# Kernel optimization log

Hardware: AMD Instinct MI355X
Metric: run time of the kernel (lower is better)

## Reference

```python
import jax, jax.numpy as jnp
import numpy as np

D_MODEL = 256
MLP_DIM = 1024
EPS = 1e-5

def _layernorm(x, g, b):
    mu = jnp.mean(x, axis=-1, keepdims=True)
    var = jnp.mean(jnp.square(x - mu), axis=-1, keepdims=True)
    return (x - mu) * jax.lax.rsqrt(var + EPS) * g + b

def setup_inputs() -> dict:
    key = jax.random.key(0)
    ks = jax.random.split(key, 4)
    d, m = D_MODEL, MLP_DIM
    x = jax.random.normal(ks[0], (8, 1024, 4, d), dtype=jnp.float32)
    w_qkv = jax.random.normal(ks[1], (3 * d, d), dtype=jnp.float32) * 0.05  # torch Linear weight (out,in)
    gamma1 = jnp.ones((d,), jnp.float32)
    beta1 = jnp.zeros((d,), jnp.float32)
    gamma2 = jnp.ones((d,), jnp.float32)
    beta2 = jnp.zeros((d,), jnp.float32)
    w1 = jax.random.normal(ks[2], (m, d), dtype=jnp.float32) * 0.05
    b1 = jnp.zeros((m,), jnp.float32)
    w2 = jax.random.normal(ks[3], (d, m), dtype=jnp.float32) * 0.05
    b2 = jnp.zeros((d,), jnp.float32)
    return {"x": x, "w_qkv": w_qkv, "gamma1": gamma1, "beta1": beta1,
            "gamma2": gamma2, "beta2": beta2, "w1": w1, "b1": b1, "w2": w2, "b2": b2}

def reference(x, w_qkv, gamma1, beta1, gamma2, beta2, w1, b1, w2, b2):
    bsz, n, h, d = x.shape
    scale = d ** -0.5
    # --- attention branch: x + attn(norm1(x)) ---
    xn = _layernorm(x, gamma1, beta1)
    # Linear(d, 3d): xn @ W^T, then reshape trailing 3d -> (d, 3) as in torch
    qkv = jnp.einsum('bnhd,ed->bnhe', xn, w_qkv).reshape(bsz, n * h, d, 3)
    q, k, v = qkv[..., 0], qkv[..., 1], qkv[..., 2]   # [b, n*h, d]
    dots = jnp.einsum('bid,bjd->bij', q, k) * scale   # [b, n*h, n*h]
    attn = jax.nn.softmax(dots, axis=-1)              # dropout=0 -> identity
    out = jnp.einsum('bij,bjd->bid', attn, v).reshape(bsz, n, h, d)
    x = x + out
    # --- mlp branch: x + mlp(norm2(x)) ---
    xn2 = _layernorm(x, gamma2, beta2)
    hid = jax.nn.silu(jnp.einsum('bnhd,md->bnhm', xn2, w1) + b1)
    x = x + jnp.einsum('bnhm,dm->bnhd', hid, w2) + b2
    return x
```

## Files before the change

### kernel.cpp

```cpp
#include <hip/hip_runtime.h>


typedef __attribute__((ext_vector_type(8))) short bf16x8;
typedef __attribute__((ext_vector_type(4))) short bf16x4;
typedef __attribute__((ext_vector_type(4))) float f32x4;
typedef __attribute__((ext_vector_type(16))) float f32x16;

static __device__ __forceinline__ short f2bf(float f) {
    union { float f; unsigned u; } v; v.f = f;
    unsigned r = (v.u + 0x7FFFu + ((v.u >> 16) & 1u)) >> 16;
    return (short)r;
}

static __device__ __forceinline__ void gll16(const void* g, void* l) {
    __builtin_amdgcn_global_load_lds(
        (const __attribute__((address_space(1))) unsigned*)g,
        (__attribute__((address_space(3))) unsigned*)l, 16, 0, 0);
}

__global__ __launch_bounds__(256) void k_cvt(const float* __restrict__ wqkv,
                                             const float* __restrict__ w1,
                                             const float* __restrict__ w2,
                                             short* __restrict__ owqkv,
                                             short* __restrict__ ow1,
                                             short* __restrict__ ow2) {
    int i = blockIdx.x * 256 + threadIdx.x;
    if (i < 196608) {
        int e = i >> 8, col = i & 255;
        int dd = e / 3, which = e - dd * 3;
        float v = wqkv[i];
        if (which == 0) v *= 0.0625f * 1.44269504f;
        owqkv[((which << 8) + dd) * 256 + col] = f2bf(v);
    }
    if (i < 262144) { ow1[i] = f2bf(w1[i]); ow2[i] = f2bf(w2[i]); }
}

__global__ __launch_bounds__(256) void k_ln(const float* __restrict__ x,
                                            const float* __restrict__ g,
                                            const float* __restrict__ bta,
                                            short* __restrict__ out) {
    int w = threadIdx.x >> 6, lane = threadIdx.x & 63;
    long row = (long)blockIdx.x * 4 + w;
    float4 v = *((const float4*)(x + row * 256) + lane);
    float s = v.x + v.y + v.z + v.w;
    float q = v.x * v.x + v.y * v.y + v.z * v.z + v.w * v.w;
    for (int off = 1; off < 64; off <<= 1) {
        s += __shfl_xor(s, off);
        q += __shfl_xor(q, off);
    }
    float mean = s * (1.0f / 256.0f);
    float var = q * (1.0f / 256.0f) - mean * mean;
    float rstd = rsqrtf(var + 1e-5f);
    float4 gg = *((const float4*)g + lane);
    float4 bb = *((const float4*)bta + lane);
    short4 o;
    o.x = f2bf((v.x - mean) * rstd * gg.x + bb.x);
    o.y = f2bf((v.y - mean) * rstd * gg.y + bb.y);
    o.z = f2bf((v.z - mean) * rstd * gg.z + bb.z);
    o.w = f2bf((v.w - mean) * rstd * gg.w + bb.w);
    *((short4*)(out + row * 256) + lane) = o;
}

__global__ __launch_bounds__(256) void k_qkv(const short* __restrict__ xn,
                                             const short* __restrict__ wb,
                                             short* __restrict__ Q,
                                             short* __restrict__ K,
                                             short* __restrict__ VT) {
    __shared__ __attribute__((aligned(16))) short lds_a[64 * 264];
    __shared__ __attribute__((aligned(16))) short lds_b[64 * 264];
    int t = threadIdx.x;
    int m0 = blockIdx.y * 64, n0 = blockIdx.x * 64;
    const int4* ga = (const int4*)xn;
    const int4* gb = (const int4*)wb;
    int4* la = (int4*)lds_a;
    int4* lb = (int4*)lds_b;
    for (int it = 0; it < 8; it++) {
        int c = t + 256 * it;
        int r = c >> 5, k = c & 31;
        la[r * 33 + k] = ga[(long)(m0 + r) * 32 + k];
        lb[r * 33 + k] = gb[(n0 + r) * 32 + k];
    }
    __syncthreads();
    int w = t >> 6, lane = t & 63, ln = lane & 15, qd = lane >> 4;
    int moff = (w >> 1) * 32, noff = (w & 1) * 32;
    f32x4 acc[2][2] = {};
    for (int ks = 0; ks < 8; ks++) {
        bf16x8 a0 = *(const bf16x8*)&lds_a[(moff + ln) * 264 + ks * 32 + qd * 8];
        bf16x8 a1 = *(const bf16x8*)&lds_a[(moff + 16 + ln) * 264 + ks * 32 + qd * 8];
        bf16x8 b0 = *(const bf16x8*)&lds_b[(noff + ln) * 264 + ks * 32 + qd * 8];
        bf16x8 b1 = *(const bf16x8*)&lds_b[(noff + 16 + ln) * 264 + ks * 32 + qd * 8];
        acc[0][0] = __builtin_amdgcn_mfma_f32_16x16x32_bf16(a0, b0, acc[0][0], 0, 0, 0);
        acc[0][1] = __builtin_amdgcn_mfma_f32_16x16x32_bf16(a0, b1, acc[0][1], 0, 0, 0);
        acc[1][0] = __builtin_amdgcn_mfma_f32_16x16x32_bf16(a1, b0, acc[1][0], 0, 0, 0);
        acc[1][1] = __builtin_amdgcn_mfma_f32_16x16x32_bf16(a1, b1, acc[1][1], 0, 0, 0);
    }
    for (int mi = 0; mi < 2; mi++)
        for (int nj = 0; nj < 2; nj++)
            for (int rg = 0; rg < 4; rg++) {
                float v = acc[mi][nj][rg];
                int gr = m0 + moff + mi * 16 + qd * 4 + rg;
                int e = n0 + noff + nj * 16 + ln;
                int which = e >> 8, dd = e & 255;
                short bv = f2bf(v);
                if (which == 0) Q[(long)gr * 256 + dd] = bv;
                else if (which == 1) K[(long)gr * 256 + dd] = bv;
                else {
                    int b = gr >> 12, i = gr & 4095;
                    VT[((long)b * 256 + dd) * 4096 + i] = bv;
                }
            }
}

__global__ __launch_bounds__(256, 1) void k_attn(const short* __restrict__ Q,
                                                 const short* __restrict__ K,
                                                 const short* __restrict__ VT,
                                                 const float* __restrict__ x,
                                                 float* __restrict__ out) {
    __shared__ __attribute__((aligned(16))) short lds_k[2][32 * 256];
    __shared__ __attribute__((aligned(16))) short lds_v[2][256 * 32];
    int t = threadIdx.x, w = t >> 6, l = t & 63, l5 = l & 31, h = l >> 5;
    int b = blockIdx.y;
    int q0 = blockIdx.x * 128 + w * 32;

    bf16x8 qf[16];
    {
        const short* qrow = Q + ((long)(b * 4096 + q0 + l5)) * 256;
        #pragma unroll
        for (int kc = 0; kc < 16; kc++) qf[kc] = *(const bf16x8*)(qrow + kc * 16 + h * 8);
    }
    f32x16 O[8] = {};
    float lsum = 0.f;

    const char* Kb = (const char*)(K + (long)b * 4096 * 256);
    const int4* gv = (const int4*)(VT + (long)b * 4096 * 256);

    long koff[4]; int klds[4];
    #pragma unroll
    for (int i = 0; i < 4; i++) {
        int r = w * 8 + i * 2 + (l >> 5);
        koff[i] = (long)r * 512 + (long)((l5 ^ (r & 31)) * 16);
        klds[i] = (w * 8 + i * 2) * 512;
    }
    int4 vs[4];

    #pragma unroll
    for (int i = 0; i < 4; i++) {
        int c = t + 256 * i;
        vs[i] = gv[(c >> 2) * 512 + (c & 3)];
    }
    #pragma unroll
    for (int i = 0; i < 4; i++) gll16(Kb + koff[i], (char*)lds_k[0] + klds[i]);
    #pragma unroll
    for (int i = 0; i < 4; i++) {
        int c = t + 256 * i, d = c >> 2, ch = c & 3;
        char* base = (char*)lds_v[0] + d * 64;
        *(int2*)(base + (((ch * 2 + 0) ^ (d & 7)) * 8)) = make_int2(vs[i].x, vs[i].y);
        *(int2*)(base + (((ch * 2 + 1) ^ (d & 7)) * 8)) = make_int2(vs[i].z, vs[i].w);
    }
    __syncthreads();

    for (int jt = 0; jt < 128; jt++) {
        int cur = jt & 1;
        if (jt < 127) {
            #pragma unroll
            for (int i = 0; i < 4; i++) {
                int c = t + 256 * i;
                vs[i] = gv[(c >> 2) * 512 + (jt + 1) * 4 + (c & 3)];
            }
            long ka = (long)(jt + 1) * 16384;
            #pragma unroll
            for (int i = 0; i < 4; i++)
                gll16(Kb + ka + koff[i], (char*)lds_k[cur ^ 1] + klds[i]);
        }
        const short* lk = lds_k[cur];
        const short* lv = lds_v[cur];
        f32x16 st = {};
        #pragma unroll
        for (int kc = 0; kc < 16; kc++) {
            int cc = kc * 2 + h;
            bf16x8 a = *(const bf16x8*)(lk + (l5 * 32 + (cc ^ l5)) * 8);
            st = __builtin_amdgcn_mfma_f32_32x32x16_bf16(a, qf[kc], st, 0, 0, 0);
        }
        bf16x4 pf[4];
        #pragma unroll
        for (int r4 = 0; r4 < 4; r4++) {
            float p0 = __builtin_amdgcn_exp2f(st[r4 * 4 + 0]);
            float p1 = __builtin_amdgcn_exp2f(st[r4 * 4 + 1]);
            float p2 = __builtin_amdgcn_exp2f(st[r4 * 4 + 2]);
            float p3 = __builtin_amdgcn_exp2f(st[r4 * 4 + 3]);
            lsum += (p0 + p1) + (p2 + p3);
            union { float f; unsigned u; } u0, u1, u2, u3;
            u0.f = p0; u1.f = p1; u2.f = p2; u3.f = p3;
            union { unsigned u[2]; bf16x4 v; } pk;
            pk.u[0] = __builtin_amdgcn_perm(u1.u + 0x8000u, u0.u + 0x8000u, 0x07060302u);
            pk.u[1] = __builtin_amdgcn_perm(u3.u + 0x8000u, u2.u + 0x8000u, 0x07060302u);
            pf[r4] = pk.v;
        }
        #pragma unroll
        for (int dt = 0; dt < 8; dt++) {
            int d = dt * 32 + l5;
            const char* vbase = (const char*)lv + d * 64;
            #pragma unroll
            for (int k4 = 0; k4 < 4; k4++) {
                bf16x4 va = *(const bf16x4*)(vbase + (((k4 * 2 + h) ^ (d & 7)) * 8));
                O[dt] = __builtin_amdgcn_mfma_f32_32x32x8bf16_1k(va, pf[k4], O[dt], 0, 0, 0);
            }
        }
        if (jt < 127) {
            #pragma unroll
            for (int i = 0; i < 4; i++) {
                int c = t + 256 * i, d = c >> 2, ch = c & 3;
                char* base = (char*)lds_v[cur ^ 1] + d * 64;
                *(int2*)(base + (((ch * 2 + 0) ^ (d & 7)) * 8)) = make_int2(vs[i].x, vs[i].y);
                *(int2*)(base + (((ch * 2 + 1) ^ (d & 7)) * 8)) = make_int2(vs[i].z, vs[i].w);
            }
        }
        __syncthreads();
    }

    float lt = lsum + __shfl_xor(lsum, 32);
    float rinv = 1.0f / lt;
    float* fscr = (float*)lds_k[0] + w * (32 * 33);
    #pragma unroll
    for (int dt = 0; dt < 8; dt++) {
        #pragma unroll
        for (int r = 0; r < 16; r++) {
            int drow = (r & 3) + 8 * (r >> 2) + 4 * h;
            fscr[drow * 33 + l5] = O[dt][r] * rinv;
        }
        asm volatile("s_waitcnt lgkmcnt(0)" ::: "memory");
        #pragma unroll
        for (int it = 0; it < 16; it++) {
            int ql = it * 2 + h;
            float v = fscr[l5 * 33 + ql];
            long idx = ((long)(b * 4096 + q0 + ql)) * 256 + dt * 32 + l5;
            out[idx] = x[idx] + v;
        }
        asm volatile("s_waitcnt lgkmcnt(0)" ::: "memory");
    }
}

__global__ __launch_bounds__(256) void k_mlp(const short* __restrict__ xn,
                                             const short* __restrict__ w1b,
                                             const short* __restrict__ w2b,
                                             const float* __restrict__ b1,
                                             const float* __restrict__ b2,
                                             float* __restrict__ out) {
    __shared__ __attribute__((aligned(16))) short lds_w[2][16 * 256];
    __shared__ __attribute__((aligned(16))) short lds_h[4][16 * 264];
    int t = threadIdx.x, w = t >> 6, l = t & 63, ln = l & 15, qd = l >> 4;
    int R0 = blockIdx.x * 64 + w * 16;
    short* lhs = lds_h[w];

    bf16x8 a1f[8];
    #pragma unroll
    for (int kc = 0; kc < 8; kc++)
        a1f[kc] = *(const bf16x8*)(xn + (long)(R0 + ln) * 256 + kc * 32 + qd * 8);

    int rr[2]; long s1off[2], s2off[2]; int wlds[2];
    #pragma unroll
    for (int i = 0; i < 2; i++) {
        int r = w * 4 + i * 2 + (l >> 5);
        int ch = (l & 31) ^ r;
        rr[i] = r;
        s1off[i] = (long)r * 512 + ch * 16;
        s2off[i] = (long)r * 2048 + ch * 16;
        wlds[i] = (w * 4 + i * 2) * 512;
    }
    const char* W1c = (const char*)w1b;
    const char* W2c = (const char*)w2b;

    f32x4 Oc[16] = {};
    #pragma unroll
    for (int i = 0; i < 2; i++)
        gll16(W1c + s1off[i], (char*)lds_w[0] + wlds[i]);
    __syncthreads();
    int cur = 0;

    for (int pass = 0; pass < 4; pass++) {
        for (int nt = 0; nt < 16; nt++) {
            if (nt < 15) {
                long base = (long)(pass * 256 + (nt + 1) * 16) * 512;
                #pragma unroll
                for (int i = 0; i < 2; i++)
                    gll16(W1c + base + s1off[i], (char*)lds_w[cur ^ 1] + wlds[i]);
            } else {
                long base = (long)pass * 512;
                #pragma unroll
                for (int i = 0; i < 2; i++)
                    gll16(W2c + base + s2off[i], (char*)lds_w[cur ^ 1] + wlds[i]);
            }
            f32x4 acc = {};
            const short* lw = lds_w[cur];
            #pragma unroll
            for (int kc = 0; kc < 8; kc++) {
                int cc = kc * 4 + qd;
                bf16x8 bf = *(const bf16x8*)(lw + (ln * 32 + (cc ^ ln)) * 8);
                acc = __builtin_amdgcn_mfma_f32_16x16x32_bf16(a1f[kc], bf, acc, 0, 0, 0);
            }
            float bb = b1[pass * 256 + nt * 16 + ln];
            #pragma unroll
            for (int rg = 0; rg < 4; rg++) {
                float z = acc[rg] + bb;
                float sv = z / (1.0f + __expf(-z));
                lhs[(qd * 4 + rg) * 264 + nt * 16 + ln] = f2bf(sv);
            }
            __syncthreads();
            cur ^= 1;
        }
        bf16x8 a2f[8];
        #pragma unroll
        for (int kc = 0; kc < 8; kc++)
            a2f[kc] = *(const bf16x8*)&lhs[ln * 264 + kc * 32 + qd * 8];
        for (int nt = 0; nt < 16; nt++) {
            if (nt < 15) {
                long base = (long)((nt + 1) * 16) * 2048 + (long)pass * 512;
                #pragma unroll
                for (int i = 0; i < 2; i++)
                    gll16(W2c + base + s2off[i], (char*)lds_w[cur ^ 1] + wlds[i]);
            } else if (pass < 3) {
                long base = (long)((pass + 1) * 256) * 512;
                #pragma unroll
                for (int i = 0; i < 2; i++)
                    gll16(W1c + base + s1off[i], (char*)lds_w[cur ^ 1] + wlds[i]);
            }
            const short* lw = lds_w[cur];
            #pragma unroll
            for (int kc = 0; kc < 8; kc++) {
                int cc = kc * 4 + qd;
                bf16x8 bf = *(const bf16x8*)(lw + (ln * 32 + (cc ^ ln)) * 8);
                Oc[nt] = __builtin_amdgcn_mfma_f32_16x16x32_bf16(a2f[kc], bf, Oc[nt], 0, 0, 0);
            }
            __syncthreads();
            cur ^= 1;
        }
    }
    for (int nt = 0; nt < 16; nt++) {
        int dd = nt * 16 + ln;
        float bb = b2[dd];
        #pragma unroll
        for (int rg = 0; rg < 4; rg++) {
            long idx = (long)(R0 + qd * 4 + rg) * 256 + dd;
            out[idx] = out[idx] + Oc[nt][rg] + bb;
        }
    }
}

extern "C" void kernel_launch(void* const* d_in, const int* in_sizes, int n_in,
                              void* d_out, int out_size, void* d_ws, size_t ws_size,
                              hipStream_t stream) {
    const float* x    = (const float*)d_in[0];
    const float* wqkv = (const float*)d_in[1];
    const float* g1   = (const float*)d_in[2];
    const float* be1  = (const float*)d_in[3];
    const float* g2   = (const float*)d_in[4];
    const float* be2  = (const float*)d_in[5];
    const float* w1   = (const float*)d_in[6];
    const float* b1   = (const float*)d_in[7];
    const float* w2   = (const float*)d_in[8];
    const float* b2   = (const float*)d_in[9];
    float* out = (float*)d_out;
    char* ws = (char*)d_ws;
    short* WQKV = (short*)(ws);
    short* W1B  = (short*)(ws + (512l << 10));
    short* W2B  = (short*)(ws + (1l << 20));
    short* XN   = (short*)(ws + (2l << 20));
    short* Qb   = (short*)(ws + (18l << 20));
    short* Kb   = (short*)(ws + (34l << 20));
    short* VTb  = (short*)(ws + (50l << 20));

    k_cvt<<<1024, 256, 0, stream>>>(wqkv, w1, w2, WQKV, W1B, W2B);
    k_ln<<<8192, 256, 0, stream>>>(x, g1, be1, XN);
    k_qkv<<<dim3(12, 512), 256, 0, stream>>>(XN, WQKV, Qb, Kb, VTb);
    k_attn<<<dim3(32, 8), 256, 0, stream>>>(Qb, Kb, VTb, x, out);
    k_ln<<<8192, 256, 0, stream>>>(out, g2, be2, XN);
    k_mlp<<<512, 256, 0, stream>>>(XN, W1B, W2B, b1, b2, out);
}
```

Measured before the change: 474.9 us.

## Split attention keys across two blocks, double Q rows per block, add merge kernel

```diff
diff --git a/kernel.cpp b/kernel.cpp
--- a/kernel.cpp
+++ b/kernel.cpp
@@ -114,130 +114,159 @@
 __global__ __launch_bounds__(256, 1) void k_attn(const short* __restrict__ Q,
                                                  const short* __restrict__ K,
                                                  const short* __restrict__ VT,
-                                                 const float* __restrict__ x,
-                                                 float* __restrict__ out) {
+                                                 float* __restrict__ Opart,
+                                                 float* __restrict__ lpart) {
     __shared__ __attribute__((aligned(16))) short lds_k[2][32 * 256];
-    __shared__ __attribute__((aligned(16))) short lds_v[2][256 * 32];
+    __shared__ __attribute__((aligned(16))) short lds_v[2][256 * 64 / 2];
     int t = threadIdx.x, w = t >> 6, l = t & 63, l5 = l & 31, h = l >> 5;
+    int qt = blockIdx.x >> 1, sp = blockIdx.x & 1;
     int b = blockIdx.y;
-    int q0 = blockIdx.x * 128 + w * 32;
-
-    bf16x8 qf[16];
-    {
-        const short* qrow = Q + ((long)(b * 4096 + q0 + l5)) * 256;
-        #pragma unroll
-        for (int kc = 0; kc < 16; kc++) qf[kc] = *(const bf16x8*)(qrow + kc * 16 + h * 8);
-    }
-    f32x16 O[8] = {};
-    float lsum = 0.f;
-
-    const char* Kb = (const char*)(K + (long)b * 4096 * 256);
-    const int4* gv = (const int4*)(VT + (long)b * 4096 * 256);
-
-    long koff[4]; int klds[4];
+    int q0 = qt * 256 + w * 32;
+
+    bf16x8 qf[2][16];
+    #pragma unroll
+    for (int r = 0; r < 2; r++) {
+        const short* qrow = Q + ((long)(b * 4096 + q0 + r * 128 + l5)) * 256;
+        #pragma unroll
+        for (int kc = 0; kc < 16; kc++)
+            qf[r][kc] = *(const bf16x8*)(qrow + kc * 16 + h * 8);
+    }
+    f32x16 O[2][8] = {};
+    float ls0 = 0.f, ls1 = 0.f;
+
+    const char* Kb = (const char*)K + ((long)(b * 4096 + sp * 2048)) * 512;
+    const char* Vb = (const char*)VT + (long)b * 256 * 8192 + (long)sp * 4096;
+
+    int koff[4];
     #pragma unroll
     for (int i = 0; i < 4; i++) {
-        int r = w * 8 + i * 2 + (l >> 5);
-        koff[i] = (long)r * 512 + (long)((l5 ^ (r & 31)) * 16);
-        klds[i] = (w * 8 + i * 2) * 512;
-    }
-    int4 vs[4];
-
+        int r = w * 8 + i * 2 + h;
+        koff[i] = r * 512 + ((l5 ^ r) * 16);
+    }
+    int voff[4];
     #pragma unroll
     for (int i = 0; i < 4; i++) {
-        int c = t + 256 * i;
-        vs[i] = gv[(c >> 2) * 512 + (c & 3)];
-    }
-    #pragma unroll
-    for (int i = 0; i < 4; i++) gll16(Kb + koff[i], (char*)lds_k[0] + klds[i]);
-    #pragma unroll
-    for (int i = 0; i < 4; i++) {
-        int c = t + 256 * i, d = c >> 2, ch = c & 3;
-        char* base = (char*)lds_v[0] + d * 64;
-        *(int2*)(base + (((ch * 2 + 0) ^ (d & 7)) * 8)) = make_int2(vs[i].x, vs[i].y);
-        *(int2*)(base + (((ch * 2 + 1) ^ (d & 7)) * 8)) = make_int2(vs[i].z, vs[i].w);
-    }
+        int s = w * 256 + i * 64 + l;
+        int d = s >> 2;
+        int k4 = (s & 3) ^ ((d >> 1) & 3);
+        voff[i] = d * 8192 + k4 * 16;
+    }
+    int xl = (l5 >> 1) & 3;
+
+    #pragma unroll
+    for (int i = 0; i < 4; i++)
+        gll16(Kb + koff[i], (char*)lds_k[0] + (w * 8 + i * 2) * 512);
+    #pragma unroll
+    for (int i = 0; i < 4; i++)
+        gll16(Vb + voff[i], (char*)lds_v[0] + (w * 256 + i * 64) * 16);
     __syncthreads();
 
-    for (int jt = 0; jt < 128; jt++) {
+    for (int jt = 0; jt < 64; jt++) {
         int cur = jt & 1;
-        if (jt < 127) {
-            #pragma unroll
-            for (int i = 0; i < 4; i++) {
-                int c = t + 256 * i;
-                vs[i] = gv[(c >> 2) * 512 + (jt + 1) * 4 + (c & 3)];
-            }
+        if (jt < 63) {
             long ka = (long)(jt + 1) * 16384;
+            long va = (long)(jt + 1) * 64;
             #pragma unroll
             for (int i = 0; i < 4; i++)
-                gll16(Kb + ka + koff[i], (char*)lds_k[cur ^ 1] + klds[i]);
+                gll16(Kb + ka + koff[i], (char*)lds_k[cur ^ 1] + (w * 8 + i * 2) * 512);
+            #pragma unroll
+            for (int i = 0; i < 4; i++)
+                gll16(Vb + va + voff[i], (char*)lds_v[cur ^ 1] + (w * 256 + i * 64) * 16);
         }
         const short* lk = lds_k[cur];
-        const short* lv = lds_v[cur];
-        f32x16 st = {};
+        const char* lv = (const char*)lds_v[cur];
+        f32x16 st0 = {}, st1 = {};
         #pragma unroll
         for (int kc = 0; kc < 16; kc++) {
             int cc = kc * 2 + h;
             bf16x8 a = *(const bf16x8*)(lk + (l5 * 32 + (cc ^ l5)) * 8);
-            st = __builtin_amdgcn_mfma_f32_32x32x16_bf16(a, qf[kc], st, 0, 0, 0);
-        }
-        bf16x4 pf[4];
+            st0 = __builtin_amdgcn_mfma_f32_32x32x16_bf16(a, qf[0][kc], st0, 0, 0, 0);
+            st1 = __builtin_amdgcn_mfma_f32_32x32x16_bf16(a, qf[1][kc], st1, 0, 0, 0);
+        }
+        bf16x4 pf0[4], pf1[4];
         #pragma unroll
         for (int r4 = 0; r4 < 4; r4++) {
-            float p0 = __builtin_amdgcn_exp2f(st[r4 * 4 + 0]);
-            float p1 = __builtin_amdgcn_exp2f(st[r4 * 4 + 1]);
-            float p2 = __builtin_amdgcn_exp2f(st[r4 * 4 + 2]);
-            float p3 = __builtin_amdgcn_exp2f(st[r4 * 4 + 3]);
-            lsum += (p0 + p1) + (p2 + p3);
-            union { float f; unsigned u; } u0, u1, u2, u3;
-            u0.f = p0; u1.f = p1; u2.f = p2; u3.f = p3;
+            float a0 = __builtin_amdgcn_exp2f(st0[r4 * 4 + 0]);
+            float a1 = __builtin_amdgcn_exp2f(st0[r4 * 4 + 1]);
+            float a2 = __builtin_amdgcn_exp2f(st0[r4 * 4 + 2]);
+            float a3 = __builtin_amdgcn_exp2f(st0[r4 * 4 + 3]);
+            ls0 += (a0 + a1) + (a2 + a3);
+            union { float f; unsigned u; } x0, x1, x2, x3;
+            x0.f = a0; x1.f = a1; x2.f = a2; x3.f = a3;
             union { unsigned u[2]; bf16x4 v; } pk;
-            pk.u[0] = __builtin_amdgcn_perm(u1.u + 0x8000u, u0.u + 0x8000u, 0x07060302u);
-            pk.u[1] = __builtin_amdgcn_perm(u3.u + 0x8000u, u2.u + 0x8000u, 0x07060302u);
-            pf[r4] = pk.v;
+            pk.u[0] = __builtin_amdgcn_perm(x1.u + 0x8000u, x0.u + 0x8000u, 0x07060302u);
+            pk.u[1] = __builtin_amdgcn_perm(x3.u + 0x8000u, x2.u + 0x8000u, 0x07060302u);
+            pf0[r4] = pk.v;
+            float b0 = __builtin_amdgcn_exp2f(st1[r4 * 4 + 0]);
+            float b1 = __builtin_amdgcn_exp2f(st1[r4 * 4 + 1]);
+            float b2 = __builtin_amdgcn_exp2f(st1[r4 * 4 + 2]);
+            float b3 = __builtin_amdgcn_exp2f(st1[r4 * 4 + 3]);
+            ls1 += (b0 + b1) + (b2 + b3);
+            x0.f = b0; x1.f = b1; x2.f = b2; x3.f = b3;
+            pk.u[0] = __builtin_amdgcn_perm(x1.u + 0x8000u, x0.u + 0x8000u, 0x07060302u);
+            pk.u[1] = __builtin_amdgcn_perm(x3.u + 0x8000u, x2.u + 0x8000u, 0x07060302u);
+            pf1[r4] = pk.v;
         }
         #pragma unroll
         for (int dt = 0; dt < 8; dt++) {
             int d = dt * 32 + l5;
-            const char* vbase = (const char*)lv + d * 64;
+            const char* vrow = lv + d * 64;
             #pragma unroll
             for (int k4 = 0; k4 < 4; k4++) {
-                bf16x4 va = *(const bf16x4*)(vbase + (((k4 * 2 + h) ^ (d & 7)) * 8));
-                O[dt] = __builtin_amdgcn_mfma_f32_32x32x8bf16_1k(va, pf[k4], O[dt], 0, 0, 0);
-            }
-        }
-        if (jt < 127) {
-            #pragma unroll
-            for (int i = 0; i < 4; i++) {
-                int c = t + 256 * i, d = c >> 2, ch = c & 3;
-                char* base = (char*)lds_v[cur ^ 1] + d * 64;
-                *(int2*)(base + (((ch * 2 + 0) ^ (d & 7)) * 8)) = make_int2(vs[i].x, vs[i].y);
-                *(int2*)(base + (((ch * 2 + 1) ^ (d & 7)) * 8)) = make_int2(vs[i].z, vs[i].w);
+                bf16x4 va = *(const bf16x4*)(vrow + ((k4 ^ xl) * 16 + h * 8));
+                O[0][dt] = __builtin_amdgcn_mfma_f32_32x32x8bf16_1k(va, pf0[k4], O[0][dt], 0, 0, 0);
+                O[1][dt] = __builtin_amdgcn_mfma_f32_32x32x8bf16_1k(va, pf1[k4], O[1][dt], 0, 0, 0);
             }
         }
         __syncthreads();
     }
 
-    float lt = lsum + __shfl_xor(lsum, 32);
-    float rinv = 1.0f / lt;
+    long obase = ((long)(sp * 8 + b)) * 4096 * 256;
+    long lbase = (long)(sp * 8 + b) * 4096;
     float* fscr = (float*)lds_k[0] + w * (32 * 33);
     #pragma unroll
-    for (int dt = 0; dt < 8; dt++) {
-        #pragma unroll
-        for (int r = 0; r < 16; r++) {
-            int drow = (r & 3) + 8 * (r >> 2) + 4 * h;
-            fscr[drow * 33 + l5] = O[dt][r] * rinv;
-        }
-        asm volatile("s_waitcnt lgkmcnt(0)" ::: "memory");
-        #pragma unroll
-        for (int it = 0; it < 16; it++) {
-            int ql = it * 2 + h;
-            float v = fscr[l5 * 33 + ql];
-            long idx = ((long)(b * 4096 + q0 + ql)) * 256 + dt * 32 + l5;
-            out[idx] = x[idx] + v;
-        }
-        asm volatile("s_waitcnt lgkmcnt(0)" ::: "memory");
-    }
+    for (int r = 0; r < 2; r++) {
+        float lsv = r ? ls1 : ls0;
+        float lt = lsv + __shfl_xor(lsv, 32);
+        int qb = q0 + r * 128;
+        if (h == 0) lpart[lbase + qb + l5] = lt;
+        #pragma unroll
+        for (int dt = 0; dt < 8; dt++) {
+            #pragma unroll
+            for (int rg = 0; rg < 16; rg++) {
+                int drow = (rg & 3) + 8 * (rg >> 2) + 4 * h;
+                fscr[drow * 33 + l5] = O[r][dt][rg];
+            }
+            asm volatile("s_waitcnt lgkmcnt(0)" ::: "memory");
+            #pragma unroll
+            for (int it = 0; it < 16; it++) {
+                int ql = it * 2 + h;
+                float v = fscr[l5 * 33 + ql];
+                Opart[obase + (long)(qb + ql) * 256 + dt * 32 + l5] = v;
+            }
+            asm volatile("s_waitcnt lgkmcnt(0)" ::: "memory");
+        }
+    }
+}
+
+__global__ __launch_bounds__(256) void k_merge(const float* __restrict__ x,
+                                               const float* __restrict__ Op,
+                                               const float* __restrict__ lp,
+                                               float* __restrict__ out) {
+    long i4 = (long)blockIdx.x * 256 + threadIdx.x;
+    long i = i4 * 4;
+    int row = (int)(i >> 8);
+    float li = lp[row] + lp[32768 + row];
+    float rinv = 1.0f / li;
+    float4 a = *(const float4*)(Op + i);
+    float4 bq = *(const float4*)(Op + (long)8 * 4096 * 256 + i);
+    float4 xx = *(const float4*)(x + i);
+    float4 o;
+    o.x = xx.x + (a.x + bq.x) * rinv;
+    o.y = xx.y + (a.y + bq.y) * rinv;
+    o.z = xx.z + (a.z + bq.z) * rinv;
+    o.w = xx.w + (a.w + bq.w) * rinv;
+    *(float4*)(out + i) = o;
 }
 
 __global__ __launch_bounds__(256) void k_mlp(const short* __restrict__ xn,
@@ -257,12 +286,11 @@
     for (int kc = 0; kc < 8; kc++)
         a1f[kc] = *(const bf16x8*)(xn + (long)(R0 + ln) * 256 + kc * 32 + qd * 8);
 
-    int rr[2]; long s1off[2], s2off[2]; int wlds[2];
+    long s1off[2], s2off[2]; int wlds[2];
     #pragma unroll
     for (int i = 0; i < 2; i++) {
         int r = w * 4 + i * 2 + (l >> 5);
         int ch = (l & 31) ^ r;
-        rr[i] = r;
         s1off[i] = (long)r * 512 + ch * 16;
         s2off[i] = (long)r * 2048 + ch * 16;
         wlds[i] = (w * 4 + i * 2) * 512;
@@ -361,18 +389,21 @@
     const float* b2   = (const float*)d_in[9];
     float* out = (float*)d_out;
     char* ws = (char*)d_ws;
-    short* WQKV = (short*)(ws);
-    short* W1B  = (short*)(ws + (512l << 10));
-    short* W2B  = (short*)(ws + (1l << 20));
-    short* XN   = (short*)(ws + (2l << 20));
-    short* Qb   = (short*)(ws + (18l << 20));
-    short* Kb   = (short*)(ws + (34l << 20));
-    short* VTb  = (short*)(ws + (50l << 20));
+    short* WQKV  = (short*)(ws);
+    short* W1B   = (short*)(ws + (512l << 10));
+    short* W2B   = (short*)(ws + (1l << 20));
+    short* XN    = (short*)(ws + (2l << 20));
+    short* Qb    = (short*)(ws + (18l << 20));
+    short* Kb    = (short*)(ws + (34l << 20));
+    short* VTb   = (short*)(ws + (50l << 20));
+    float* Opart = (float*)(ws + (66l << 20));
+    float* lpart = (float*)(ws + (130l << 20));
 
     k_cvt<<<1024, 256, 0, stream>>>(wqkv, w1, w2, WQKV, W1B, W2B);
     k_ln<<<8192, 256, 0, stream>>>(x, g1, be1, XN);
     k_qkv<<<dim3(12, 512), 256, 0, stream>>>(XN, WQKV, Qb, Kb, VTb);
-    k_attn<<<dim3(32, 8), 256, 0, stream>>>(Qb, Kb, VTb, x, out);
+    k_attn<<<dim3(32, 8), 256, 0, stream>>>(Qb, Kb, VTb, Opart, lpart);
+    k_merge<<<8192, 256, 0, stream>>>(x, Opart, lpart, out);
     k_ln<<<8192, 256, 0, stream>>>(out, g2, be2, XN);
     k_mlp<<<512, 256, 0, stream>>>(XN, W1B, W2B, b1, b2, out);
 }
```

New measurement: 980.6 us. 2.06x slower.

## Load V tiles via direct global-to-LDS with new swizzle; split QK accumulator

Applied to the files above, without the earlier changes.

```diff
diff --git a/kernel.cpp b/kernel.cpp
--- a/kernel.cpp
+++ b/kernel.cpp
@@ -132,55 +132,56 @@
     float lsum = 0.f;
 
     const char* Kb = (const char*)(K + (long)b * 4096 * 256);
-    const int4* gv = (const int4*)(VT + (long)b * 4096 * 256);
-
-    long koff[4]; int klds[4];
+    const char* Vb = (const char*)(VT + (long)b * 256 * 4096);
+
+    int koff[4];
     #pragma unroll
     for (int i = 0; i < 4; i++) {
-        int r = w * 8 + i * 2 + (l >> 5);
-        koff[i] = (long)r * 512 + (long)((l5 ^ (r & 31)) * 16);
-        klds[i] = (w * 8 + i * 2) * 512;
-    }
-    int4 vs[4];
-
+        int r = w * 8 + i * 2 + h;
+        koff[i] = r * 512 + ((l5 ^ r) * 16);
+    }
+    int voff[4];
     #pragma unroll
     for (int i = 0; i < 4; i++) {
-        int c = t + 256 * i;
-        vs[i] = gv[(c >> 2) * 512 + (c & 3)];
-    }
-    #pragma unroll
-    for (int i = 0; i < 4; i++) gll16(Kb + koff[i], (char*)lds_k[0] + klds[i]);
-    #pragma unroll
-    for (int i = 0; i < 4; i++) {
-        int c = t + 256 * i, d = c >> 2, ch = c & 3;
-        char* base = (char*)lds_v[0] + d * 64;
-        *(int2*)(base + (((ch * 2 + 0) ^ (d & 7)) * 8)) = make_int2(vs[i].x, vs[i].y);
-        *(int2*)(base + (((ch * 2 + 1) ^ (d & 7)) * 8)) = make_int2(vs[i].z, vs[i].w);
-    }
+        int s = w * 256 + i * 64 + l;
+        int d = s >> 2;
+        int m = (s & 3) ^ ((d >> 1) & 3);
+        voff[i] = d * 8192 + m * 16;
+    }
+    int xl = (l5 >> 1) & 3;
+
+    #pragma unroll
+    for (int i = 0; i < 4; i++)
+        gll16(Kb + koff[i], (char*)lds_k[0] + (w * 8 + i * 2) * 512);
+    #pragma unroll
+    for (int i = 0; i < 4; i++)
+        gll16(Vb + voff[i], (char*)lds_v[0] + (w * 256 + i * 64) * 16);
     __syncthreads();
 
     for (int jt = 0; jt < 128; jt++) {
         int cur = jt & 1;
         if (jt < 127) {
-            #pragma unroll
-            for (int i = 0; i < 4; i++) {
-                int c = t + 256 * i;
-                vs[i] = gv[(c >> 2) * 512 + (jt + 1) * 4 + (c & 3)];
-            }
             long ka = (long)(jt + 1) * 16384;
+            long va = (long)(jt + 1) * 64;
             #pragma unroll
             for (int i = 0; i < 4; i++)
-                gll16(Kb + ka + koff[i], (char*)lds_k[cur ^ 1] + klds[i]);
+                gll16(Kb + ka + koff[i], (char*)lds_k[cur ^ 1] + (w * 8 + i * 2) * 512);
+            #pragma unroll
+            for (int i = 0; i < 4; i++)
+                gll16(Vb + va + voff[i], (char*)lds_v[cur ^ 1] + (w * 256 + i * 64) * 16);
         }
         const short* lk = lds_k[cur];
-        const short* lv = lds_v[cur];
-        f32x16 st = {};
-        #pragma unroll
-        for (int kc = 0; kc < 16; kc++) {
-            int cc = kc * 2 + h;
-            bf16x8 a = *(const bf16x8*)(lk + (l5 * 32 + (cc ^ l5)) * 8);
-            st = __builtin_amdgcn_mfma_f32_32x32x16_bf16(a, qf[kc], st, 0, 0, 0);
-        }
+        const char* lv = (const char*)lds_v[cur];
+        f32x16 sta = {}, stb = {};
+        #pragma unroll
+        for (int kc = 0; kc < 16; kc += 2) {
+            int c0 = kc * 2 + h, c1 = (kc + 1) * 2 + h;
+            bf16x8 a0 = *(const bf16x8*)(lk + (l5 * 32 + (c0 ^ l5)) * 8);
+            bf16x8 a1 = *(const bf16x8*)(lk + (l5 * 32 + (c1 ^ l5)) * 8);
+            sta = __builtin_amdgcn_mfma_f32_32x32x16_bf16(a0, qf[kc], sta, 0, 0, 0);
+            stb = __builtin_amdgcn_mfma_f32_32x32x16_bf16(a1, qf[kc + 1], stb, 0, 0, 0);
+        }
+        f32x16 st = sta + stb;
         bf16x4 pf[4];
         #pragma unroll
         for (int r4 = 0; r4 < 4; r4++) {
@@ -199,20 +200,11 @@
         #pragma unroll
         for (int dt = 0; dt < 8; dt++) {
             int d = dt * 32 + l5;
-            const char* vbase = (const char*)lv + d * 64;
+            const char* vrow = lv + d * 64;
             #pragma unroll
             for (int k4 = 0; k4 < 4; k4++) {
-                bf16x4 va = *(const bf16x4*)(vbase + (((k4 * 2 + h) ^ (d & 7)) * 8));
+                bf16x4 va = *(const bf16x4*)(vrow + ((k4 ^ xl) * 16 + h * 8));
                 O[dt] = __builtin_amdgcn_mfma_f32_32x32x8bf16_1k(va, pf[k4], O[dt], 0, 0, 0);
-            }
-        }
-        if (jt < 127) {
-            #pragma unroll
-            for (int i = 0; i < 4; i++) {
-                int c = t + 256 * i, d = c >> 2, ch = c & 3;
-                char* base = (char*)lds_v[cur ^ 1] + d * 64;
-                *(int2*)(base + (((ch * 2 + 0) ^ (d & 7)) * 8)) = make_int2(vs[i].x, vs[i].y);
-                *(int2*)(base + (((ch * 2 + 1) ^ (d & 7)) * 8)) = make_int2(vs[i].z, vs[i].w);
             }
         }
         __syncthreads();
@@ -257,12 +249,11 @@
     for (int kc = 0; kc < 8; kc++)
         a1f[kc] = *(const bf16x8*)(xn + (long)(R0 + ln) * 256 + kc * 32 + qd * 8);
 
-    int rr[2]; long s1off[2], s2off[2]; int wlds[2];
+    long s1off[2], s2off[2]; int wlds[2];
     #pragma unroll
     for (int i = 0; i < 2; i++) {
         int r = w * 4 + i * 2 + (l >> 5);
         int ch = (l & 31) ^ r;
-        rr[i] = r;
         s1off[i] = (long)r * 512 + ch * 16;
         s2off[i] = (long)r * 2048 + ch * 16;
         wlds[i] = (w * 4 + i * 2) * 512;
```

New measurement: 487.7 us. 1.03x slower.
